# Kernel optimization log

Hardware: AMD Instinct MI355X
Metric: run time of the kernel (lower is better)

Reference implementation:

```python
import math
import jax, jax.numpy as jnp
import numpy as np

NUM_HEADS = 16
BASE = 10000.0


def _rope_sin_cos(seq_len, head_dim):
    # theta_j = pos / base^(2j/dim), j in [0, dim//2)
    j = jnp.arange(head_dim // 2, dtype=jnp.float32)
    inv_freq = jnp.power(jnp.float32(BASE), -2.0 * j / head_dim)  # [d/2]
    pos = jnp.arange(seq_len, dtype=jnp.float32)
    ang = pos[:, None] * inv_freq[None, :]          # [S, d/2]
    sin, cos = jnp.sin(ang), jnp.cos(ang)
    # interleave-repeat each entry twice: [S, d]
    sin2 = jnp.stack([sin, sin], axis=-1).reshape(seq_len, head_dim)
    cos2 = jnp.stack([cos, cos], axis=-1).reshape(seq_len, head_dim)
    return sin2, cos2


def _apply_rope(x, sin2, cos2):
    # x: [B, H, S, d]; rotate-half interleaved: (-x1, x0, -x3, x2, ...)
    x_even, x_odd = x[..., 0::2], x[..., 1::2]
    rot = jnp.stack([-x_odd, x_even], axis=-1).reshape(x.shape)
    return x * cos2 + rot * sin2


def setup_inputs() -> dict:
    key = jax.random.key(0)
    ks = jax.random.split(key, 9)
    B, S, H = 2, 2048, 2048
    sc = 1.0 / math.sqrt(H)
    return {
        "hidden_state": jax.random.normal(ks[0], (B, S, H), jnp.float32),
        "Wq": jax.random.normal(ks[1], (H, H), jnp.float32) * sc,
        "bq": jax.random.normal(ks[2], (H,), jnp.float32) * 0.01,
        "Wk": jax.random.normal(ks[3], (H, H), jnp.float32) * sc,
        "bk": jax.random.normal(ks[4], (H,), jnp.float32) * 0.01,
        "Wv": jax.random.normal(ks[5], (H, H), jnp.float32) * sc,
        "bv": jax.random.normal(ks[6], (H,), jnp.float32) * 0.01,
        "Wo": jax.random.normal(ks[7], (H, H), jnp.float32) * sc,
        "bo": jax.random.normal(ks[8], (H,), jnp.float32) * 0.01,
    }


def reference(hidden_state, Wq, bq, Wk, bk, Wv, bv, Wo, bo):
    B, S, H = hidden_state.shape
    nh = NUM_HEADS
    hd = H // nh

    def proj(W, b):
        y = jnp.einsum('bsh,hd->bsd', hidden_state, W) + b
        return y.reshape(B, S, nh, hd).transpose(0, 2, 1, 3)  # [B,nh,S,hd]

    q = proj(Wq, bq)
    k = proj(Wk, bk)
    v = proj(Wv, bv)

    sin2, cos2 = _rope_sin_cos(S, hd)  # [S, hd]
    q = _apply_rope(q, sin2, cos2)
    k = _apply_rope(k, sin2, cos2)

    scale = 1.0 / math.sqrt(hd)
    attn = jnp.einsum('bhqd,bhkd->bhqk', q, k) * scale  # [B,nh,S,S]
    attn = jax.nn.softmax(attn, axis=-1)
    out = jnp.einsum('bhqk,bhkd->bhqd', attn, v)
    out = out.transpose(0, 2, 1, 3).reshape(B, S, H)
    return jnp.einsum('bsh,hd->bsd', out, Wo) + bo
```

## Files before the change

kernel.cpp:

```cpp
#include <hip/hip_runtime.h>
#include <math.h>


typedef __bf16 bf16;
typedef __attribute__((ext_vector_type(8))) __bf16 bf16x8;
typedef __attribute__((ext_vector_type(4))) __bf16 bf16x4;
typedef __attribute__((ext_vector_type(4))) float f32x4;

#define S_LEN 2048
#define NHEAD 16
#define HD 128

__device__ __forceinline__ void async16(const void* g, void* l) {
    __builtin_amdgcn_global_load_lds(
        (const __attribute__((address_space(1))) void*)g,
        (__attribute__((address_space(3))) void*)l, 16, 0, 0);
}

__device__ __forceinline__ f32x4 mfma16(bf16x8 a, bf16x8 b, f32x4 c) {
    return __builtin_amdgcn_mfma_f32_16x16x32_bf16(a, b, c, 0, 0, 0);
}

__global__ __launch_bounds__(256) void cvt_f32_bf16(const float* __restrict__ x,
                                                    bf16* __restrict__ y, int n) {
    int i = (blockIdx.x * 256 + threadIdx.x) * 4;
    if (i + 3 < n) {
        const float4 v = *(const float4*)(x + i);
        bf16x4 o;
        o[0] = (bf16)v.x; o[1] = (bf16)v.y; o[2] = (bf16)v.z; o[3] = (bf16)v.w;
        *(bf16x4*)(y + i) = o;
    }
}

__global__ __launch_bounds__(128) void rope_tables(float* __restrict__ st,
                                                   float* __restrict__ ct) {
    const int s = blockIdx.x, d = threadIdx.x;
    const float invf = exp2f(-0.20762050593046013f * (float)(d >> 1));
    float sn, cs;
    sincosf((float)s * invf, &sn, &cs);
    st[(s << 7) | d] = sn;
    ct[(s << 7) | d] = cs;
}

__global__ __launch_bounds__(256) void transpose_cvt(const float* __restrict__ W,
                                                     bf16* __restrict__ Wt,
                                                     int Kd, int Nd) {
    __shared__ float tile[32][33];
    const int tx = threadIdx.x & 31, ty = threadIdx.x >> 5;
    const int bn = blockIdx.x * 32, bk = blockIdx.y * 32;
#pragma unroll
    for (int r = 0; r < 32; r += 8)
        tile[ty + r][tx] = W[(size_t)(bk + ty + r) * Nd + bn + tx];
    __syncthreads();
#pragma unroll
    for (int r = 0; r < 32; r += 8)
        Wt[(size_t)(bn + ty + r) * Kd + bk + tx] = (bf16)tile[tx][ty + r];
}

__global__ __launch_bounds__(256, 2)
void gemm_qkv(const bf16* __restrict__ A, const bf16* __restrict__ Bt,
              const float* __restrict__ bq, const float* __restrict__ bk,
              const float* __restrict__ bv, bf16* __restrict__ Qo,
              bf16* __restrict__ Ko, bf16* __restrict__ Vo,
              const float* __restrict__ stab, const float* __restrict__ ctab) {
    const int K = 2048;
    __shared__ __align__(16) bf16 smem[17408];
    bf16* As = smem;
    bf16* Bs = smem + 8192;
    const int t = threadIdx.x;
    const int w = t >> 6, l = t & 63;
    const int lr = l & 15, lq = l >> 4;
    const int m0 = blockIdx.y * 128, n0 = blockIdx.x * 128;
    const int wm = (w >> 1) * 64, wn = (w & 1) * 64;
    const int seg = n0 >> 11;
    const float* bias = (seg == 0) ? bq : (seg == 1) ? bk : bv;
    bf16* outB = (seg == 0) ? Qo : (seg == 1) ? Ko : Vo;

    f32x4 acc[4][4];
    const f32x4 fz = {0.f, 0.f, 0.f, 0.f};
#pragma unroll
    for (int i = 0; i < 4; ++i)
#pragma unroll
        for (int j = 0; j < 4; ++j) acc[i][j] = fz;

    for (int k0 = 0; k0 < K; k0 += 64) {
        __syncthreads();
#pragma unroll
        for (int c = 0; c < 4; ++c) {
            const int chunk = c * 256 + t;
            const int row = chunk >> 3, kc = (chunk & 7) << 3;
            async16(A + (size_t)(m0 + row) * K + k0 + kc, &As[chunk * 8]);
            async16(Bt + (size_t)(n0 + row) * K + k0 + kc, &Bs[chunk * 8]);
        }
        __syncthreads();
#pragma unroll
        for (int s = 0; s < 2; ++s) {
            bf16x8 af[4], bfr[4];
#pragma unroll
            for (int i = 0; i < 4; ++i)
                af[i] = *(const bf16x8*)&As[(wm + i * 16 + lr) * 64 + s * 32 + lq * 8];
#pragma unroll
            for (int j = 0; j < 4; ++j)
                bfr[j] = *(const bf16x8*)&Bs[(wn + j * 16 + lr) * 64 + s * 32 + lq * 8];
#pragma unroll
            for (int i = 0; i < 4; ++i)
#pragma unroll
                for (int j = 0; j < 4; ++j)
                    acc[i][j] = mfma16(af[i], bfr[j], acc[i][j]);
        }
    }

    if (seg == 2) {
        __syncthreads();
#pragma unroll
        for (int i = 0; i < 4; ++i) {
            const int rl0 = wm + i * 16 + lq * 4;
#pragma unroll
            for (int j = 0; j < 4; ++j) {
                const int cl = wn + j * 16 + lr;
                const float bv_ = bias[(n0 & 2047) + cl];
#pragma unroll
                for (int r = 0; r < 4; ++r)
                    smem[cl * 136 + rl0 + r] = (bf16)(acc[i][j][r] + bv_);
            }
        }
        __syncthreads();
        const int b = m0 >> 11;
#pragma unroll
        for (int p = 0; p < 8; ++p) {
            const int idx = p * 256 + t;
            const int col = idx >> 4, ch = idx & 15;
            const bf16x8 v = *(const bf16x8*)&smem[col * 136 + ch * 8];
            const int cg2 = (n0 & 2047) + col;
            const int h = cg2 >> 7, d = cg2 & 127;
            *(bf16x8*)&outB[((size_t)((b << 4) | h) * HD + d) * S_LEN +
                            (m0 & 2047) + ch * 8] = v;
        }
    } else {
#pragma unroll
        for (int i = 0; i < 4; ++i) {
            const int rg0 = m0 + wm + i * 16 + lq * 4;
#pragma unroll
            for (int j = 0; j < 4; ++j) {
                const int cg2 = (n0 & 2047) + wn + j * 16 + lr;
                const float bv_ = bias[cg2];
                const int h = cg2 >> 7, d = cg2 & 127;
#pragma unroll
                for (int r = 0; r < 4; ++r) {
                    const int rg = rg0 + r;
                    const int b = rg >> 11, s = rg & 2047;
                    float v = acc[i][j][r] + bv_;
                    float p = __shfl_xor(v, 1);
                    const float sn = stab[(s << 7) | d];
                    const float cs = ctab[(s << 7) | d];
                    float o = (d & 1) ? (v * cs + p * sn) : (v * cs - p * sn);
                    if (seg == 0) o *= 0.08838834764831843f;
                    outB[((size_t)((b << 4) + h) * S_LEN + s) * HD + d] = (bf16)o;
                }
            }
        }
    }
}

__global__ __launch_bounds__(256, 2)
void gemm_out(const bf16* __restrict__ A, const bf16* __restrict__ Bt,
              const float* __restrict__ bias, float* __restrict__ outF,
              int M, int N, int K) {
    __shared__ __align__(16) bf16 As[128 * 64];
    __shared__ __align__(16) bf16 Bs[128 * 64];
    const int t = threadIdx.x;
    const int w = t >> 6, l = t & 63;
    const int lr = l & 15, lq = l >> 4;
    const int m0 = blockIdx.y * 128, n0 = blockIdx.x * 128;
    const int wm = (w >> 1) * 64, wn = (w & 1) * 64;

    f32x4 acc[4][4];
    const f32x4 fz = {0.f, 0.f, 0.f, 0.f};
#pragma unroll
    for (int i = 0; i < 4; ++i)
#pragma unroll
        for (int j = 0; j < 4; ++j) acc[i][j] = fz;

    for (int k0 = 0; k0 < K; k0 += 64) {
        __syncthreads();
#pragma unroll
        for (int c = 0; c < 4; ++c) {
            const int chunk = c * 256 + t;
            const int row = chunk >> 3, kc = (chunk & 7) << 3;
            async16(A + (size_t)(m0 + row) * K + k0 + kc, &As[chunk * 8]);
            async16(Bt + (size_t)(n0 + row) * K + k0 + kc, &Bs[chunk * 8]);
        }
        __syncthreads();
#pragma unroll
        for (int s = 0; s < 2; ++s) {
            bf16x8 af[4], bfr[4];
#pragma unroll
            for (int i = 0; i < 4; ++i)
                af[i] = *(const bf16x8*)&As[(wm + i * 16 + lr) * 64 + s * 32 + lq * 8];
#pragma unroll
            for (int j = 0; j < 4; ++j)
                bfr[j] = *(const bf16x8*)&Bs[(wn + j * 16 + lr) * 64 + s * 32 + lq * 8];
#pragma unroll
            for (int i = 0; i < 4; ++i)
#pragma unroll
                for (int j = 0; j < 4; ++j)
                    acc[i][j] = mfma16(af[i], bfr[j], acc[i][j]);
        }
    }
#pragma unroll
    for (int i = 0; i < 4; ++i) {
        const int rg0 = m0 + wm + i * 16 + lq * 4;
#pragma unroll
        for (int j = 0; j < 4; ++j) {
            const int cg = n0 + wn + j * 16 + lr;
            const float bv = bias[cg];
#pragma unroll
            for (int r = 0; r < 4; ++r)
                outF[(size_t)(rg0 + r) * N + cg] = acc[i][j][r] + bv;
        }
    }
}

__global__ __launch_bounds__(256, 2)
void attn_fwd(const bf16* __restrict__ Q, const bf16* __restrict__ K,
              const bf16* __restrict__ Vt, bf16* __restrict__ AO) {
    __shared__ __align__(16) bf16 Ks[64 * 128];
    __shared__ __align__(16) bf16 Vs[128 * 64];
    const int t = threadIdx.x;
    const int w = t >> 6, l = t & 63;
    const int lr = l & 15, lq = l >> 4;
    const int blk = blockIdx.x;
    const int qt = (blk >> 3) & 15;
    const int bh = ((blk & 7) << 2) | (blk >> 7);
    const int b = bh >> 4, h = bh & 15;

    const bf16* Qp = Q + (size_t)bh * S_LEN * HD;
    const bf16* Kp = K + (size_t)bh * S_LEN * HD;
    const bf16* Vp = Vt + (size_t)bh * HD * S_LEN;

    bf16x8 qf[2][4];
#pragma unroll
    for (int i = 0; i < 2; ++i)
#pragma unroll
        for (int s = 0; s < 4; ++s)
            qf[i][s] = *(const bf16x8*)&Qp[(size_t)(qt * 128 + w * 32 + i * 16 + lr) * HD +
                                           s * 32 + lq * 8];

    f32x4 O[2][8];
    const f32x4 fz = {0.f, 0.f, 0.f, 0.f};
#pragma unroll
    for (int i = 0; i < 2; ++i)
#pragma unroll
        for (int jd = 0; jd < 8; ++jd) O[i][jd] = fz;
    float lst[2][4] = {{0.f, 0.f, 0.f, 0.f}, {0.f, 0.f, 0.f, 0.f}};

    bf16x8 rK[4], rV[4];
#pragma unroll
    for (int c = 0; c < 4; ++c) {
        const int chunk = c * 256 + t;
        const int kr = chunk >> 4, kc = chunk & 15;
        const int vr = chunk >> 3, vc = chunk & 7;
        rK[c] = *(const bf16x8*)&Kp[(size_t)kr * HD + kc * 8];
        rV[c] = *(const bf16x8*)&Vp[(size_t)vr * S_LEN + vc * 8];
    }

    for (int kt = 0; kt < 32; ++kt) {
#pragma unroll
        for (int c = 0; c < 4; ++c) {
            const int chunk = c * 256 + t;
            const int kr = chunk >> 4, kc = chunk & 15;
            const int vr = chunk >> 3, vc = chunk & 7;
            *(bf16x8*)&Ks[(kr * 16 + (kc ^ (kr & 15))) * 8] = rK[c];
            *(bf16x8*)&Vs[(vr * 8 + (vc ^ (vr & 7))) * 8] = rV[c];
        }
        __syncthreads();

        if (kt < 31) {
#pragma unroll
            for (int c = 0; c < 4; ++c) {
                const int chunk = c * 256 + t;
                const int kr = chunk >> 4, kc = chunk & 15;
                const int vr = chunk >> 3, vc = chunk & 7;
                rK[c] = *(const bf16x8*)&Kp[(size_t)((kt + 1) * 64 + kr) * HD + kc * 8];
                rV[c] = *(const bf16x8*)&Vp[(size_t)vr * S_LEN + (kt + 1) * 64 + vc * 8];
            }
        }

        f32x4 Sc[2][4];
#pragma unroll
        for (int i = 0; i < 2; ++i)
#pragma unroll
            for (int j = 0; j < 4; ++j) Sc[i][j] = fz;
#pragma unroll
        for (int s = 0; s < 4; ++s) {
            bf16x8 kf[4];
#pragma unroll
            for (int j = 0; j < 4; ++j) {
                const int krow = j * 16 + lr;
                kf[j] = *(const bf16x8*)&Ks[(krow * 16 + ((s * 4 + lq) ^ (krow & 15))) * 8];
            }
#pragma unroll
            for (int i = 0; i < 2; ++i)
#pragma unroll
                for (int j = 0; j < 4; ++j)
                    Sc[i][j] = mfma16(qf[i][s], kf[j], Sc[i][j]);
        }
        __syncthreads();

        bf16* Ps = Ks;
#pragma unroll
        for (int i = 0; i < 2; ++i)
#pragma unroll
            for (int j = 0; j < 4; ++j)
#pragma unroll
                for (int r = 0; r < 4; ++r) {
                    const float p = __expf(Sc[i][j][r]);
                    lst[i][r] += p;
                    const int prow = w * 32 + i * 16 + lq * 4 + r;
                    const int pch = (j * 2 + (lr >> 3)) ^ (prow & 7);
                    Ps[(prow * 8 + pch) * 8 + (lr & 7)] = (bf16)p;
                }

#pragma unroll
        for (int s = 0; s < 2; ++s) {
            bf16x8 pf[2], vf[8];
#pragma unroll
            for (int i = 0; i < 2; ++i) {
                const int prow = w * 32 + i * 16 + lr;
                pf[i] = *(const bf16x8*)&Ps[(prow * 8 + ((s * 4 + lq) ^ (prow & 7))) * 8];
            }
#pragma unroll
            for (int jd = 0; jd < 8; ++jd) {
                const int vrow = jd * 16 + lr;
                vf[jd] = *(const bf16x8*)&Vs[(vrow * 8 + ((s * 4 + lq) ^ (vrow & 7))) * 8];
            }
#pragma unroll
            for (int i = 0; i < 2; ++i)
#pragma unroll
                for (int jd = 0; jd < 8; ++jd)
                    O[i][jd] = mfma16(pf[i], vf[jd], O[i][jd]);
        }
        __syncthreads();
    }

#pragma unroll
    for (int mask = 1; mask < 16; mask <<= 1)
#pragma unroll
        for (int i = 0; i < 2; ++i)
#pragma unroll
            for (int r = 0; r < 4; ++r) lst[i][r] += __shfl_xor(lst[i][r], mask);

#pragma unroll
    for (int i = 0; i < 2; ++i)
#pragma unroll
        for (int jd = 0; jd < 8; ++jd)
#pragma unroll
            for (int r = 0; r < 4; ++r) {
                const int srow = qt * 128 + w * 32 + i * 16 + lq * 4 + r;
                const float v = O[i][jd][r] / lst[i][r];
                AO[(size_t)(b * S_LEN + srow) * 2048 + h * HD + jd * 16 + lr] = (bf16)v;
            }
}

extern "C" void kernel_launch(void* const* d_in, const int* in_sizes, int n_in,
                              void* d_out, int out_size, void* d_ws, size_t ws_size,
                              hipStream_t stream) {
    const float* hs = (const float*)d_in[0];
    const float* Wq = (const float*)d_in[1];
    const float* bq = (const float*)d_in[2];
    const float* Wk = (const float*)d_in[3];
    const float* bk = (const float*)d_in[4];
    const float* Wv = (const float*)d_in[5];
    const float* bv = (const float*)d_in[6];
    const float* Wo = (const float*)d_in[7];
    const float* bo = (const float*)d_in[8];
    float* out = (float*)d_out;

    char* ws = (char*)d_ws;
    bf16* Xb = (bf16*)ws;
    bf16* Wt3 = (bf16*)(ws + (size_t)16777216);
    bf16* Qb = (bf16*)(ws + (size_t)41943040);
    bf16* Kb = (bf16*)(ws + (size_t)58720256);
    bf16* Vb = (bf16*)(ws + (size_t)75497472);
    float* stab = (float*)(ws + (size_t)92274688);
    float* ctab = (float*)(ws + (size_t)93323264);
    bf16* AO = Xb;

    const dim3 tg(64, 64);

    rope_tables<<<2048, 128, 0, stream>>>(stab, ctab);
    cvt_f32_bf16<<<8192, 256, 0, stream>>>(hs, Xb, 8388608);
    transpose_cvt<<<tg, 256, 0, stream>>>(Wq, Wt3, 2048, 2048);
    transpose_cvt<<<tg, 256, 0, stream>>>(Wk, Wt3 + (size_t)2048 * 2048, 2048, 2048);
    transpose_cvt<<<tg, 256, 0, stream>>>(Wv, Wt3 + (size_t)2 * 2048 * 2048, 2048, 2048);
    gemm_qkv<<<dim3(48, 32), 256, 0, stream>>>(Xb, Wt3, bq, bk, bv, Qb, Kb, Vb,
                                               stab, ctab);
    attn_fwd<<<512, 256, 0, stream>>>(Qb, Kb, Vb, AO);
    transpose_cvt<<<tg, 256, 0, stream>>>(Wo, Wt3, 2048, 2048);
    gemm_out<<<dim3(16, 32), 256, 0, stream>>>(AO, Wt3, bo, out, 4096, 2048, 2048);
}
```

Before: 426.8 us.

## Register-prefetch GEMM tiles with XOR-swizzled LDS layout and higher occupancy

Both projection GEMMs stop using direct global-to-LDS async loads. They now prefetch the next K-tile into registers while the current tile is consumed, then store it into LDS with an XOR swizzle on the 16-byte chunk index to avoid bank conflicts on the MFMA fragment reads. Launch bounds rise from 2 to 3 blocks per CU to allow more waves. The register staging adds VGPR pressure, which may conflict with the higher occupancy target and cause spills.

```diff
diff --git a/kernel.cpp b/kernel.cpp
--- a/kernel.cpp
+++ b/kernel.cpp
@@ -10,12 +10,6 @@
 #define S_LEN 2048
 #define NHEAD 16
 #define HD 128
-
-__device__ __forceinline__ void async16(const void* g, void* l) {
-    __builtin_amdgcn_global_load_lds(
-        (const __attribute__((address_space(1))) void*)g,
-        (__attribute__((address_space(3))) void*)l, 16, 0, 0);
-}
 
 __device__ __forceinline__ f32x4 mfma16(bf16x8 a, bf16x8 b, f32x4 c) {
     return __builtin_amdgcn_mfma_f32_16x16x32_bf16(a, b, c, 0, 0, 0);
@@ -57,7 +51,7 @@
         Wt[(size_t)(bn + ty + r) * Kd + bk + tx] = (bf16)tile[tx][ty + r];
 }
 
-__global__ __launch_bounds__(256, 2)
+__global__ __launch_bounds__(256, 3)
 void gemm_qkv(const bf16* __restrict__ A, const bf16* __restrict__ Bt,
               const float* __restrict__ bq, const float* __restrict__ bk,
               const float* __restrict__ bv, bf16* __restrict__ Qo,
@@ -83,35 +77,57 @@
 #pragma unroll
         for (int j = 0; j < 4; ++j) acc[i][j] = fz;
 
+    bf16x8 rA[4], rB[4];
+#pragma unroll
+    for (int c = 0; c < 4; ++c) {
+        const int chunk = c * 256 + t;
+        const int row = chunk >> 3, cc = chunk & 7;
+        rA[c] = *(const bf16x8*)&A[(size_t)(m0 + row) * K + cc * 8];
+        rB[c] = *(const bf16x8*)&Bt[(size_t)(n0 + row) * K + cc * 8];
+    }
+
     for (int k0 = 0; k0 < K; k0 += 64) {
-        __syncthreads();
 #pragma unroll
         for (int c = 0; c < 4; ++c) {
             const int chunk = c * 256 + t;
-            const int row = chunk >> 3, kc = (chunk & 7) << 3;
-            async16(A + (size_t)(m0 + row) * K + k0 + kc, &As[chunk * 8]);
-            async16(Bt + (size_t)(n0 + row) * K + k0 + kc, &Bs[chunk * 8]);
-        }
-        __syncthreads();
+            const int row = chunk >> 3, cc = chunk & 7;
+            const int d = (row * 8 + (cc ^ (row & 7))) * 8;
+            *(bf16x8*)&As[d] = rA[c];
+            *(bf16x8*)&Bs[d] = rB[c];
+        }
+        __syncthreads();
+        if (k0 + 64 < K) {
+#pragma unroll
+            for (int c = 0; c < 4; ++c) {
+                const int chunk = c * 256 + t;
+                const int row = chunk >> 3, cc = chunk & 7;
+                rA[c] = *(const bf16x8*)&A[(size_t)(m0 + row) * K + k0 + 64 + cc * 8];
+                rB[c] = *(const bf16x8*)&Bt[(size_t)(n0 + row) * K + k0 + 64 + cc * 8];
+            }
+        }
 #pragma unroll
         for (int s = 0; s < 2; ++s) {
             bf16x8 af[4], bfr[4];
 #pragma unroll
-            for (int i = 0; i < 4; ++i)
-                af[i] = *(const bf16x8*)&As[(wm + i * 16 + lr) * 64 + s * 32 + lq * 8];
-#pragma unroll
-            for (int j = 0; j < 4; ++j)
-                bfr[j] = *(const bf16x8*)&Bs[(wn + j * 16 + lr) * 64 + s * 32 + lq * 8];
+            for (int i = 0; i < 4; ++i) {
+                const int row = wm + i * 16 + lr;
+                af[i] = *(const bf16x8*)&As[(row * 8 + ((s * 4 + lq) ^ (row & 7))) * 8];
+            }
+#pragma unroll
+            for (int j = 0; j < 4; ++j) {
+                const int row = wn + j * 16 + lr;
+                bfr[j] = *(const bf16x8*)&Bs[(row * 8 + ((s * 4 + lq) ^ (row & 7))) * 8];
+            }
 #pragma unroll
             for (int i = 0; i < 4; ++i)
 #pragma unroll
                 for (int j = 0; j < 4; ++j)
                     acc[i][j] = mfma16(af[i], bfr[j], acc[i][j]);
         }
+        __syncthreads();
     }
 
     if (seg == 2) {
-        __syncthreads();
 #pragma unroll
         for (int i = 0; i < 4; ++i) {
             const int rl0 = wm + i * 16 + lq * 4;
@@ -162,7 +178,7 @@
     }
 }
 
-__global__ __launch_bounds__(256, 2)
+__global__ __launch_bounds__(256, 3)
 void gemm_out(const bf16* __restrict__ A, const bf16* __restrict__ Bt,
               const float* __restrict__ bias, float* __restrict__ outF,
               int M, int N, int K) {
@@ -181,31 +197,54 @@
 #pragma unroll
         for (int j = 0; j < 4; ++j) acc[i][j] = fz;
 
+    bf16x8 rA[4], rB[4];
+#pragma unroll
+    for (int c = 0; c < 4; ++c) {
+        const int chunk = c * 256 + t;
+        const int row = chunk >> 3, cc = chunk & 7;
+        rA[c] = *(const bf16x8*)&A[(size_t)(m0 + row) * K + cc * 8];
+        rB[c] = *(const bf16x8*)&Bt[(size_t)(n0 + row) * K + cc * 8];
+    }
+
     for (int k0 = 0; k0 < K; k0 += 64) {
-        __syncthreads();
 #pragma unroll
         for (int c = 0; c < 4; ++c) {
             const int chunk = c * 256 + t;
-            const int row = chunk >> 3, kc = (chunk & 7) << 3;
-            async16(A + (size_t)(m0 + row) * K + k0 + kc, &As[chunk * 8]);
-            async16(Bt + (size_t)(n0 + row) * K + k0 + kc, &Bs[chunk * 8]);
-        }
-        __syncthreads();
+            const int row = chunk >> 3, cc = chunk & 7;
+            const int d = (row * 8 + (cc ^ (row & 7))) * 8;
+            *(bf16x8*)&As[d] = rA[c];
+            *(bf16x8*)&Bs[d] = rB[c];
+        }
+        __syncthreads();
+        if (k0 + 64 < K) {
+#pragma unroll
+            for (int c = 0; c < 4; ++c) {
+                const int chunk = c * 256 + t;
+                const int row = chunk >> 3, cc = chunk & 7;
+                rA[c] = *(const bf16x8*)&A[(size_t)(m0 + row) * K + k0 + 64 + cc * 8];
+                rB[c] = *(const bf16x8*)&Bt[(size_t)(n0 + row) * K + k0 + 64 + cc * 8];
+            }
+        }
 #pragma unroll
         for (int s = 0; s < 2; ++s) {
             bf16x8 af[4], bfr[4];
 #pragma unroll
-            for (int i = 0; i < 4; ++i)
-                af[i] = *(const bf16x8*)&As[(wm + i * 16 + lr) * 64 + s * 32 + lq * 8];
-#pragma unroll
-            for (int j = 0; j < 4; ++j)
-                bfr[j] = *(const bf16x8*)&Bs[(wn + j * 16 + lr) * 64 + s * 32 + lq * 8];
+            for (int i = 0; i < 4; ++i) {
+                const int row = wm + i * 16 + lr;
+                af[i] = *(const bf16x8*)&As[(row * 8 + ((s * 4 + lq) ^ (row & 7))) * 8];
+            }
+#pragma unroll
+            for (int j = 0; j < 4; ++j) {
+                const int row = wn + j * 16 + lr;
+                bfr[j] = *(const bf16x8*)&Bs[(row * 8 + ((s * 4 + lq) ^ (row & 7))) * 8];
+            }
 #pragma unroll
             for (int i = 0; i < 4; ++i)
 #pragma unroll
                 for (int j = 0; j < 4; ++j)
                     acc[i][j] = mfma16(af[i], bfr[j], acc[i][j]);
         }
+        __syncthreads();
     }
 #pragma unroll
     for (int i = 0; i < 4; ++i) {
```

Measured after the change: 406.0 us. -4.9%, faster.
